# Performance work log

Hardware: AMD Instinct MI355X
Metric: run time of the kernel (lower is better)

Reference implementation:

```python
import jax, jax.numpy as jnp
import numpy as np

N = 50000
E = 800000
HID = 128
NH = 8
DH = HID // NH


def setup_inputs() -> dict:
    key = jax.random.key(0)
    ks = jax.random.split(key, 12)
    h = jax.random.normal(ks[0], (N, HID), dtype=jnp.float32)
    row = jnp.sort(jax.random.randint(ks[1], (E,), 0, N))
    col = jax.random.randint(ks[2], (E,), 0, N)
    s = 1.0 / np.sqrt(HID)
    Wq = jax.random.uniform(ks[3], (HID, HID), jnp.float32, -s, s)
    bq = jax.random.uniform(ks[4], (HID,), jnp.float32, -s, s)
    Wk = jax.random.uniform(ks[5], (HID, HID), jnp.float32, -s, s)
    bk = jax.random.uniform(ks[6], (HID,), jnp.float32, -s, s)
    Wv = jax.random.uniform(ks[7], (HID, HID), jnp.float32, -s, s)
    bv = jax.random.uniform(ks[8], (HID,), jnp.float32, -s, s)
    Wo = jax.random.uniform(ks[9], (HID, HID), jnp.float32, -s, s)
    bo = jax.random.uniform(ks[10], (HID,), jnp.float32, -s, s)
    return {"h": h, "row": row, "col": col, "Wq": Wq, "bq": bq,
            "Wk": Wk, "bk": bk, "Wv": Wv, "bv": bv, "Wo": Wo, "bo": bo}


def reference(h, row, col, Wq, bq, Wk, bk, Wv, bv, Wo, bo):
    n = h.shape[0]
    # projections; torch view(N, dh, nh): heads are the fastest-varying axis
    q = (h @ Wq.T + bq).reshape(n, DH, NH)
    k = (h @ Wk.T + bk).reshape(n, DH, NH)
    v = (h @ Wv.T + bv).reshape(n, DH, NH)
    # sddmm: per-edge score[e, head] = sum_d q[row_e, d, head] * k[col_e, d, head]
    scores = jnp.einsum('edh,edh->eh', q[row], k[col]) / np.sqrt(DH)
    # sparse softmax over each row's neighbors (dim=1)
    m = jax.ops.segment_max(scores, row, num_segments=n)       # [N, nh]
    e = jnp.exp(scores - m[row])                               # [E, nh]
    z = jax.ops.segment_sum(e, row, num_segments=n)            # [N, nh]
    attn = e / z[row]
    # bspmm: out[i] = sum_{j in N(i)} attn[ij] * v[j]
    out = jax.ops.segment_sum(attn[:, None, :] * v[col], row, num_segments=n)
    out = out.reshape(n, HID)
    return out @ Wo.T + bo
```

## Files before the change

kernel.cpp:

```cpp
#include <hip/hip_runtime.h>
#include <hip/hip_bf16.h>
#include <math.h>

#define HID 128
#define NH 8
#define DH 16

typedef __bf16 bf16x8 __attribute__((ext_vector_type(8)));
typedef __bf16 bf16x4 __attribute__((ext_vector_type(4)));
typedef float  f32x4  __attribute__((ext_vector_type(4)));

__global__ void prep_kernel(const int* __restrict__ row, int* __restrict__ row_ptr,
                            int N_, int E_,
                            const float* __restrict__ Wq, const float* __restrict__ Wk,
                            const float* __restrict__ Wv, const float* __restrict__ Wo,
                            const float* __restrict__ bq, const float* __restrict__ bk,
                            const float* __restrict__ bv,
                            __bf16* __restrict__ Whi, float* __restrict__ bias384) {
    int idx = blockIdx.x * blockDim.x + threadIdx.x;
    if (idx < 4 * 16384) {
        int j = idx >> 14;
        int rem = idx & 16383;
        float x;
        if (j < 3) {
            const float* W = (j == 0) ? Wq : (j == 1) ? Wk : Wv;
            x = W[rem];
        } else {
            int o  = rem >> 7;
            int kp = rem & 127;
            int k  = ((kp & 15) << 3) | (kp >> 4);
            x = Wo[o * 128 + k];
        }
        Whi[idx] = (__bf16)x;
    }
    if (idx <= N_) {
        int lo = 0, hi = E_;
        while (lo < hi) {
            int mid = (lo + hi) >> 1;
            if (row[mid] < idx) lo = mid + 1; else hi = mid;
        }
        row_ptr[idx] = lo;
    }
    if (idx < 384) {
        int j = idx >> 7;
        int pcol = idx & 127;
        int o = ((pcol & 15) << 3) | (pcol >> 4);
        const float* b = (j == 0) ? bq : (j == 1) ? bk : bv;
        bias384[idx] = b[o];
    }
}

__global__ __launch_bounds__(256)
void qkv_mfma_kernel(const float* __restrict__ h, int M,
                     const __bf16* __restrict__ Whi,
                     const float* __restrict__ bias384,
                     __bf16* __restrict__ q, __bf16* __restrict__ kv) {
    __shared__ __bf16 As[64 * 128];
    int tid  = threadIdx.x;
    int wv   = tid >> 6;
    int lane = tid & 63;
    int r    = lane & 15;
    int kg   = lane >> 4;
    int m0   = blockIdx.x * 64;
    int by   = blockIdx.y;

    #pragma unroll
    for (int it = 0; it < 4; ++it) {
        int flat = it * 256 + tid;
        int row  = flat >> 4;
        int s    = flat & 15;
        int g    = s ^ (row & 7);
        int grow = m0 + row; if (grow > M - 1) grow = M - 1;
        const float* src = &h[(size_t)grow * 128 + g * 8];
        float4 x0 = *(const float4*)src;
        float4 x1 = *(const float4*)(src + 4);
        float xs[8] = {x0.x, x0.y, x0.z, x0.w, x1.x, x1.y, x1.z, x1.w};
        bf16x8 hv8;
        #pragma unroll
        for (int e = 0; e < 8; ++e) hv8[e] = (__bf16)xs[e];
        *(bf16x8*)&As[row * 128 + s * 8] = hv8;
    }
    __syncthreads();

    f32x4 acc[3][4];
    #pragma unroll
    for (int cf = 0; cf < 3; ++cf)
        #pragma unroll
        for (int rf = 0; rf < 4; ++rf)
            acc[cf][rf] = (f32x4){0.f, 0.f, 0.f, 0.f};

    int wrow[3], jseg[3], pcb[3];
    #pragma unroll
    for (int cf = 0; cf < 3; ++cf) {
        int fb   = wv * 48 + cf * 16;
        int seg  = fb >> 6;
        int pcol = by * 64 + (fb & 63) + r;
        int o    = ((pcol & 15) << 3) | (pcol >> 4);
        wrow[cf] = (seg * 128 + o) * 128;
        jseg[cf] = seg;
        pcb[cf]  = pcol;
    }

    #pragma unroll
    for (int t = 0; t < 4; ++t) {
        int k0   = t * 32 + kg * 8;
        int slot = t * 4 + kg;
        bf16x8 bh[3];
        #pragma unroll
        for (int cf = 0; cf < 3; ++cf)
            bh[cf] = *(const bf16x8*)&Whi[wrow[cf] + k0];
        bf16x8 ah[4];
        #pragma unroll
        for (int rf = 0; rf < 4; ++rf) {
            int row = rf * 16 + r;
            int s2  = slot ^ (r & 7);
            ah[rf] = *(bf16x8*)&As[row * 128 + s2 * 8];
        }
        #pragma unroll
        for (int cf = 0; cf < 3; ++cf)
            #pragma unroll
            for (int rf = 0; rf < 4; ++rf)
                acc[cf][rf] = __builtin_amdgcn_mfma_f32_16x16x32_bf16(ah[rf], bh[cf], acc[cf][rf], 0, 0, 0);
    }

    __syncthreads();
    __bf16* kvs = &As[0];
    int orow = kg * 4;
    #pragma unroll
    for (int cf = 0; cf < 3; ++cf) {
        int j    = jseg[cf];
        int pcol = pcb[cf];
        float b  = bias384[j * 128 + pcol];
        #pragma unroll
        for (int rf = 0; rf < 4; ++rf) {
            #pragma unroll
            for (int e = 0; e < 4; ++e) {
                int mrow = rf * 16 + orow + e;
                float val = acc[cf][rf][e] + b;
                if (j == 0) {
                    int mg = m0 + mrow;
                    if (mg < M) q[(size_t)mg * 128 + pcol] = (__bf16)val;
                } else {
                    int gl  = (pcol & 63) >> 2;
                    int idx = gl * 8 + ((j == 1) ? 0 : 4) + (pcol & 3);
                    kvs[mrow * 128 + idx] = (__bf16)val;
                }
            }
        }
    }
    __syncthreads();
    #pragma unroll
    for (int it = 0; it < 4; ++it) {
        int flat = it * 256 + tid;
        int row  = flat >> 4;
        int u    = flat & 15;
        int mg   = m0 + row;
        if (mg < M)
            *(uint4*)&kv[(size_t)mg * 256 + by * 128 + u * 8] =
                *(uint4*)&kvs[row * 128 + u * 8];
    }
}

__device__ __forceinline__ float blo(unsigned u) { return __uint_as_float(u << 16); }
__device__ __forceinline__ float bhi(unsigned u) { return __uint_as_float(u & 0xffff0000u); }

__global__ __launch_bounds__(256)
void edge_attn_kernel(const int* __restrict__ row_ptr, const int* __restrict__ col,
                      const __bf16* __restrict__ q, const __bf16* __restrict__ kv,
                      __bf16* __restrict__ ob, int N_) {
    int wave = threadIdx.x >> 6;
    int lane = threadIdx.x & 63;
    int node = blockIdx.x * 4 + wave;
    if (node >= N_) return;
    int sl   = lane & 31;
    int half = lane >> 5;

    uint2 qu = *(const uint2*)&q[(size_t)node * 128 + sl * 4];
    float qx = blo(qu.x), qy = bhi(qu.x), qz = blo(qu.y), qw = bhi(qu.y);

    int e0 = row_ptr[node];
    int e1 = row_ptr[node + 1];

    float m = -INFINITY, z = 0.f;
    float4 acc = make_float4(0.f, 0.f, 0.f, 0.f);

    auto score = [&](uint4 u) {
        float p = qx * blo(u.x) + qy * bhi(u.x) +
                  qz * blo(u.y) + qw * bhi(u.y);
        p += __shfl_xor(p, 1);
        p += __shfl_xor(p, 2);
        return p * 0.25f;
    };

    int eb = e0;
    for (; eb + 8 <= e1; eb += 8) {
        int ea = eb + half * 4;
        int c0 = col[ea], c1 = col[ea + 1], c2 = col[ea + 2], c3 = col[ea + 3];
        uint4 u0 = *(const uint4*)(kv + (size_t)c0 * 256 + sl * 8);
        uint4 u1 = *(const uint4*)(kv + (size_t)c1 * 256 + sl * 8);
        uint4 u2 = *(const uint4*)(kv + (size_t)c2 * 256 + sl * 8);
        uint4 u3 = *(const uint4*)(kv + (size_t)c3 * 256 + sl * 8);
        float s0 = score(u0), s1 = score(u1), s2 = score(u2), s3 = score(u3);
        float m03 = fmaxf(fmaxf(s0, s1), fmaxf(s2, s3));
        float w0 = __expf(s0 - m03), w1 = __expf(s1 - m03);
        float w2 = __expf(s2 - m03), w3 = __expf(s3 - m03);
        float zl = (w0 + w1) + (w2 + w3);
        float lx = w0 * blo(u0.z) + w1 * blo(u1.z) + w2 * blo(u2.z) + w3 * blo(u3.z);
        float ly = w0 * bhi(u0.z) + w1 * bhi(u1.z) + w2 * bhi(u2.z) + w3 * bhi(u3.z);
        float lz = w0 * blo(u0.w) + w1 * blo(u1.w) + w2 * blo(u2.w) + w3 * blo(u3.w);
        float lw = w0 * bhi(u0.w) + w1 * bhi(u1.w) + w2 * bhi(u2.w) + w3 * bhi(u3.w);
        float mn = fmaxf(m, m03);
        float a1 = __expf(m - mn);
        float a2 = __expf(m03 - mn);
        z = z * a1 + zl * a2;
        acc.x = acc.x * a1 + lx * a2;
        acc.y = acc.y * a1 + ly * a2;
        acc.z = acc.z * a1 + lz * a2;
        acc.w = acc.w * a1 + lw * a2;
        m = mn;
    }
    for (; eb < e1; eb += 2) {
        int my_e   = eb + half;
        bool valid = (my_e < e1);
        int cnode  = valid ? col[my_e] : col[eb];
        uint4 u = *(const uint4*)(kv + (size_t)cnode * 256 + sl * 8);
        float s = valid ? score(u) : -INFINITY;
        float mnew = fmaxf(m, s);
        if (mnew > -INFINITY) {
            float alpha = __expf(m - mnew);
            float w     = __expf(s - mnew);
            z = z * alpha + w;
            acc.x = acc.x * alpha + w * blo(u.z);
            acc.y = acc.y * alpha + w * bhi(u.z);
            acc.z = acc.z * alpha + w * blo(u.w);
            acc.w = acc.w * alpha + w * bhi(u.w);
            m = mnew;
        }
    }

    float m2 = __shfl_xor(m, 32);
    float z2 = __shfl_xor(z, 32);
    float ax = __shfl_xor(acc.x, 32);
    float ay = __shfl_xor(acc.y, 32);
    float az = __shfl_xor(acc.z, 32);
    float aw = __shfl_xor(acc.w, 32);
    float mm = fmaxf(m, m2);
    if (mm > -INFINITY) {
        float a1 = __expf(m - mm);
        float a2 = __expf(m2 - mm);
        z = z * a1 + z2 * a2;
        acc.x = acc.x * a1 + ax * a2;
        acc.y = acc.y * a1 + ay * a2;
        acc.z = acc.z * a1 + az * a2;
        acc.w = acc.w * a1 + aw * a2;
    }

    if (half == 0) {
        float inv = (z > 0.f) ? 1.0f / z : 0.f;
        bf16x4 hv4;
        hv4[0] = (__bf16)(acc.x * inv);
        hv4[1] = (__bf16)(acc.y * inv);
        hv4[2] = (__bf16)(acc.z * inv);
        hv4[3] = (__bf16)(acc.w * inv);
        *(bf16x4*)&ob[(size_t)node * 128 + sl * 4] = hv4;
    }
}

__global__ __launch_bounds__(256)
void outproj_mfma_kernel(const __bf16* __restrict__ A_g, int M,
                         const __bf16* __restrict__ Whi,
                         const float* __restrict__ bo, float* __restrict__ C) {
    __shared__ __bf16 As[64 * 128];
    int tid  = threadIdx.x;
    int wv   = tid >> 6;
    int lane = tid & 63;
    int r    = lane & 15;
    int kg   = lane >> 4;
    int m0   = blockIdx.x * 64;
    int by   = blockIdx.y;
    int col  = by * 64 + wv * 16 + r;

    #pragma unroll
    for (int it = 0; it < 4; ++it) {
        int flat = it * 256 + tid;
        int row  = flat >> 4;
        int s    = flat & 15;
        int g    = s ^ (row & 7);
        int grow = m0 + row; if (grow > M - 1) grow = M - 1;
        *(bf16x8*)&As[row * 128 + s * 8] = *(const bf16x8*)&A_g[(size_t)grow * 128 + g * 8];
    }
    __syncthreads();

    f32x4 acc[4];
    #pragma unroll
    for (int rf = 0; rf < 4; ++rf) acc[rf] = (f32x4){0.f, 0.f, 0.f, 0.f};

    int wrow = col * 128;
    #pragma unroll
    for (int t = 0; t < 4; ++t) {
        int k0   = t * 32 + kg * 8;
        int slot = t * 4 + kg;
        bf16x8 bh = *(const bf16x8*)&Whi[wrow + k0];
        bf16x8 ah[4];
        #pragma unroll
        for (int rf = 0; rf < 4; ++rf) {
            int row = rf * 16 + r;
            int s2  = slot ^ (r & 7);
            ah[rf] = *(bf16x8*)&As[row * 128 + s2 * 8];
        }
        #pragma unroll
        for (int rf = 0; rf < 4; ++rf)
            acc[rf] = __builtin_amdgcn_mfma_f32_16x16x32_bf16(ah[rf], bh, acc[rf], 0, 0, 0);
    }

    float b = bo[col];
    #pragma unroll
    for (int rf = 0; rf < 4; ++rf) {
        #pragma unroll
        for (int e = 0; e < 4; ++e) {
            int mg = m0 + rf * 16 + kg * 4 + e;
            if (mg < M) C[(size_t)mg * 128 + col] = acc[rf][e] + b;
        }
    }
}

extern "C" void kernel_launch(void* const* d_in, const int* in_sizes, int n_in,
                              void* d_out, int out_size, void* d_ws, size_t ws_size,
                              hipStream_t stream) {
    const float* h  = (const float*)d_in[0];
    const int* row  = (const int*)d_in[1];
    const int* col  = (const int*)d_in[2];
    const float* Wq = (const float*)d_in[3];
    const float* bq = (const float*)d_in[4];
    const float* Wk = (const float*)d_in[5];
    const float* bk = (const float*)d_in[6];
    const float* Wv = (const float*)d_in[7];
    const float* bv = (const float*)d_in[8];
    const float* Wo = (const float*)d_in[9];
    const float* bo = (const float*)d_in[10];
    float* out = (float*)d_out;

    int N_ = in_sizes[0] / HID;
    int E_ = in_sizes[1];

    char* ws = (char*)d_ws;
    size_t off = 0;
    auto alloc = [&](size_t bytes) {
        void* p = (void*)(ws + off);
        off = (off + bytes + 255) & ~(size_t)255;
        return p;
    };
    int*    row_ptr = (int*)   alloc((size_t)(N_ + 1) * sizeof(int));
    __bf16* qb      = (__bf16*)alloc((size_t)N_ * 128 * sizeof(__bf16));
    __bf16* kvb     = (__bf16*)alloc((size_t)N_ * 256 * sizeof(__bf16));
    __bf16* obb     = (__bf16*)alloc((size_t)N_ * 128 * sizeof(__bf16));
    __bf16* Whi     = (__bf16*)alloc((size_t)4 * 16384 * sizeof(__bf16));
    float*  bias384 = (float*) alloc(384 * sizeof(float));
    (void)ws_size;

    prep_kernel<<<256, 256, 0, stream>>>(row, row_ptr, N_, E_,
                                         Wq, Wk, Wv, Wo, bq, bk, bv,
                                         Whi, bias384);
    qkv_mfma_kernel<<<dim3((N_ + 63) / 64, 2), 256, 0, stream>>>(
        h, N_, Whi, bias384, qb, kvb);
    edge_attn_kernel<<<(N_ + 3) / 4, 256, 0, stream>>>(row_ptr, col, qb, kvb, obb, N_);
    outproj_mfma_kernel<<<dim3((N_ + 63) / 64, 2), 256, 0, stream>>>(
        obb, N_, Whi + 3 * 16384, bo, out);
}
```

Baseline: 192.2 us.

## Split interleaved KV buffer into separate K and V arrays and unify edge loop

The QKV projection now writes K and V straight to two separate row-major bf16 buffers. This drops the shared-memory staging and the interleaved 256-wide KV layout. The edge attention kernel gathers K and V with two 8-byte loads per neighbor instead of one 16-byte load, and folds the tail loop into the main 8-edge loop using clamped indices and masked scores. The aim is simpler writes and fewer syncs in the projection kernel, at the cost of two separate gathered cache lines per neighbor in the memory-bound edge kernel and wasted work on partial tail iterations.

```diff
diff --git a/kernel.cpp b/kernel.cpp
--- a/kernel.cpp
+++ b/kernel.cpp
@@ -28,8 +28,8 @@
         } else {
             int o  = rem >> 7;
             int kp = rem & 127;
-            int k  = ((kp & 15) << 3) | (kp >> 4);
-            x = Wo[o * 128 + k];
+            int kk = ((kp & 15) << 3) | (kp >> 4);
+            x = Wo[o * 128 + kk];
         }
         Whi[idx] = (__bf16)x;
     }
@@ -54,7 +54,8 @@
 void qkv_mfma_kernel(const float* __restrict__ h, int M,
                      const __bf16* __restrict__ Whi,
                      const float* __restrict__ bias384,
-                     __bf16* __restrict__ q, __bf16* __restrict__ kv) {
+                     __bf16* __restrict__ q, __bf16* __restrict__ k,
+                     __bf16* __restrict__ v) {
     __shared__ __bf16 As[64 * 128];
     int tid  = threadIdx.x;
     int wv   = tid >> 6;
@@ -123,41 +124,21 @@
                 acc[cf][rf] = __builtin_amdgcn_mfma_f32_16x16x32_bf16(ah[rf], bh[cf], acc[cf][rf], 0, 0, 0);
     }
 
-    __syncthreads();
-    __bf16* kvs = &As[0];
     int orow = kg * 4;
     #pragma unroll
     for (int cf = 0; cf < 3; ++cf) {
         int j    = jseg[cf];
         int pcol = pcb[cf];
+        __bf16* dst = (j == 0) ? q : (j == 1) ? k : v;
         float b  = bias384[j * 128 + pcol];
         #pragma unroll
         for (int rf = 0; rf < 4; ++rf) {
             #pragma unroll
             for (int e = 0; e < 4; ++e) {
-                int mrow = rf * 16 + orow + e;
-                float val = acc[cf][rf][e] + b;
-                if (j == 0) {
-                    int mg = m0 + mrow;
-                    if (mg < M) q[(size_t)mg * 128 + pcol] = (__bf16)val;
-                } else {
-                    int gl  = (pcol & 63) >> 2;
-                    int idx = gl * 8 + ((j == 1) ? 0 : 4) + (pcol & 3);
-                    kvs[mrow * 128 + idx] = (__bf16)val;
-                }
+                int mg = m0 + rf * 16 + orow + e;
+                if (mg < M) dst[(size_t)mg * 128 + pcol] = (__bf16)(acc[cf][rf][e] + b);
             }
         }
-    }
-    __syncthreads();
-    #pragma unroll
-    for (int it = 0; it < 4; ++it) {
-        int flat = it * 256 + tid;
-        int row  = flat >> 4;
-        int u    = flat & 15;
-        int mg   = m0 + row;
-        if (mg < M)
-            *(uint4*)&kv[(size_t)mg * 256 + by * 128 + u * 8] =
-                *(uint4*)&kvs[row * 128 + u * 8];
     }
 }
 
@@ -166,7 +147,8 @@
 
 __global__ __launch_bounds__(256)
 void edge_attn_kernel(const int* __restrict__ row_ptr, const int* __restrict__ col,
-                      const __bf16* __restrict__ q, const __bf16* __restrict__ kv,
+                      const __bf16* __restrict__ q, const __bf16* __restrict__ kb,
+                      const __bf16* __restrict__ vb,
                       __bf16* __restrict__ ob, int N_) {
     int wave = threadIdx.x >> 6;
     int lane = threadIdx.x & 63;
@@ -184,7 +166,7 @@
     float m = -INFINITY, z = 0.f;
     float4 acc = make_float4(0.f, 0.f, 0.f, 0.f);
 
-    auto score = [&](uint4 u) {
+    auto score = [&](uint2 u) {
         float p = qx * blo(u.x) + qy * bhi(u.x) +
                   qz * blo(u.y) + qw * bhi(u.y);
         p += __shfl_xor(p, 1);
@@ -192,49 +174,44 @@
         return p * 0.25f;
     };
 
-    int eb = e0;
-    for (; eb + 8 <= e1; eb += 8) {
-        int ea = eb + half * 4;
-        int c0 = col[ea], c1 = col[ea + 1], c2 = col[ea + 2], c3 = col[ea + 3];
-        uint4 u0 = *(const uint4*)(kv + (size_t)c0 * 256 + sl * 8);
-        uint4 u1 = *(const uint4*)(kv + (size_t)c1 * 256 + sl * 8);
-        uint4 u2 = *(const uint4*)(kv + (size_t)c2 * 256 + sl * 8);
-        uint4 u3 = *(const uint4*)(kv + (size_t)c3 * 256 + sl * 8);
-        float s0 = score(u0), s1 = score(u1), s2 = score(u2), s3 = score(u3);
+    for (int eb = e0; eb < e1; eb += 8) {
+        int ea  = eb + half * 4;
+        bool b0 = ea     < e1, b1 = ea + 1 < e1, b2 = ea + 2 < e1, b3 = ea + 3 < e1;
+        int i0 = b0 ? ea     : e1 - 1;
+        int i1 = b1 ? ea + 1 : e1 - 1;
+        int i2 = b2 ? ea + 2 : e1 - 1;
+        int i3 = b3 ? ea + 3 : e1 - 1;
+        int c0 = col[i0], c1 = col[i1], c2 = col[i2], c3 = col[i3];
+        uint2 k0 = *(const uint2*)(kb + (size_t)c0 * 128 + sl * 4);
+        uint2 k1 = *(const uint2*)(kb + (size_t)c1 * 128 + sl * 4);
+        uint2 k2 = *(const uint2*)(kb + (size_t)c2 * 128 + sl * 4);
+        uint2 k3 = *(const uint2*)(kb + (size_t)c3 * 128 + sl * 4);
+        uint2 v0 = *(const uint2*)(vb + (size_t)c0 * 128 + sl * 4);
+        uint2 v1 = *(const uint2*)(vb + (size_t)c1 * 128 + sl * 4);
+        uint2 v2 = *(const uint2*)(vb + (size_t)c2 * 128 + sl * 4);
+        uint2 v3 = *(const uint2*)(vb + (size_t)c3 * 128 + sl * 4);
+        float s0 = b0 ? score(k0) : -INFINITY;
+        float s1 = b1 ? score(k1) : -INFINITY;
+        float s2 = b2 ? score(k2) : -INFINITY;
+        float s3 = b3 ? score(k3) : -INFINITY;
         float m03 = fmaxf(fmaxf(s0, s1), fmaxf(s2, s3));
-        float w0 = __expf(s0 - m03), w1 = __expf(s1 - m03);
-        float w2 = __expf(s2 - m03), w3 = __expf(s3 - m03);
-        float zl = (w0 + w1) + (w2 + w3);
-        float lx = w0 * blo(u0.z) + w1 * blo(u1.z) + w2 * blo(u2.z) + w3 * blo(u3.z);
-        float ly = w0 * bhi(u0.z) + w1 * bhi(u1.z) + w2 * bhi(u2.z) + w3 * bhi(u3.z);
-        float lz = w0 * blo(u0.w) + w1 * blo(u1.w) + w2 * blo(u2.w) + w3 * blo(u3.w);
-        float lw = w0 * bhi(u0.w) + w1 * bhi(u1.w) + w2 * bhi(u2.w) + w3 * bhi(u3.w);
-        float mn = fmaxf(m, m03);
-        float a1 = __expf(m - mn);
-        float a2 = __expf(m03 - mn);
-        z = z * a1 + zl * a2;
-        acc.x = acc.x * a1 + lx * a2;
-        acc.y = acc.y * a1 + ly * a2;
-        acc.z = acc.z * a1 + lz * a2;
-        acc.w = acc.w * a1 + lw * a2;
-        m = mn;
-    }
-    for (; eb < e1; eb += 2) {
-        int my_e   = eb + half;
-        bool valid = (my_e < e1);
-        int cnode  = valid ? col[my_e] : col[eb];
-        uint4 u = *(const uint4*)(kv + (size_t)cnode * 256 + sl * 8);
-        float s = valid ? score(u) : -INFINITY;
-        float mnew = fmaxf(m, s);
-        if (mnew > -INFINITY) {
-            float alpha = __expf(m - mnew);
-            float w     = __expf(s - mnew);
-            z = z * alpha + w;
-            acc.x = acc.x * alpha + w * blo(u.z);
-            acc.y = acc.y * alpha + w * bhi(u.z);
-            acc.z = acc.z * alpha + w * blo(u.w);
-            acc.w = acc.w * alpha + w * bhi(u.w);
-            m = mnew;
+        if (m03 > -INFINITY) {
+            float w0 = __expf(s0 - m03), w1 = __expf(s1 - m03);
+            float w2 = __expf(s2 - m03), w3 = __expf(s3 - m03);
+            float zl = (w0 + w1) + (w2 + w3);
+            float lx = w0 * blo(v0.x) + w1 * blo(v1.x) + w2 * blo(v2.x) + w3 * blo(v3.x);
+            float ly = w0 * bhi(v0.x) + w1 * bhi(v1.x) + w2 * bhi(v2.x) + w3 * bhi(v3.x);
+            float lz = w0 * blo(v0.y) + w1 * blo(v1.y) + w2 * blo(v2.y) + w3 * blo(v3.y);
+            float lw = w0 * bhi(v0.y) + w1 * bhi(v1.y) + w2 * bhi(v2.y) + w3 * bhi(v3.y);
+            float mn = fmaxf(m, m03);
+            float a1 = __expf(m - mn);
+            float a2 = __expf(m03 - mn);
+            z = z * a1 + zl * a2;
+            acc.x = acc.x * a1 + lx * a2;
+            acc.y = acc.y * a1 + ly * a2;
+            acc.z = acc.z * a1 + lz * a2;
+            acc.w = acc.w * a1 + lw * a2;
+            m = mn;
         }
     }
 
@@ -352,7 +329,8 @@
     };
     int*    row_ptr = (int*)   alloc((size_t)(N_ + 1) * sizeof(int));
     __bf16* qb      = (__bf16*)alloc((size_t)N_ * 128 * sizeof(__bf16));
-    __bf16* kvb     = (__bf16*)alloc((size_t)N_ * 256 * sizeof(__bf16));
+    __bf16* kvk     = (__bf16*)alloc((size_t)N_ * 128 * sizeof(__bf16));
+    __bf16* kvv     = (__bf16*)alloc((size_t)N_ * 128 * sizeof(__bf16));
     __bf16* obb     = (__bf16*)alloc((size_t)N_ * 128 * sizeof(__bf16));
     __bf16* Whi     = (__bf16*)alloc((size_t)4 * 16384 * sizeof(__bf16));
     float*  bias384 = (float*) alloc(384 * sizeof(float));
@@ -362,8 +340,8 @@
                                          Wq, Wk, Wv, Wo, bq, bk, bv,
                                          Whi, bias384);
     qkv_mfma_kernel<<<dim3((N_ + 63) / 64, 2), 256, 0, stream>>>(
-        h, N_, Whi, bias384, qb, kvb);
-    edge_attn_kernel<<<(N_ + 3) / 4, 256, 0, stream>>>(row_ptr, col, qb, kvb, obb, N_);
+        h, N_, Whi, bias384, qb, kvk, kvv);
+    edge_attn_kernel<<<(N_ + 3) / 4, 256, 0, stream>>>(row_ptr, col, qb, kvk, kvv, obb, N_);
     outproj_mfma_kernel<<<dim3((N_ + 63) / 64, 2), 256, 0, stream>>>(
         obb, N_, Whi + 3 * 16384, bo, out);
 }
```

After: 198.5 us. 1.03x slower.
